# Performance work log

Measured on AMD Instinct MI355X. Metric: run time of the kernel, lower is better.

Reference implementation:

```python
import jax, jax.numpy as jnp
import numpy as np

DIM = 1024
INTER = 2048
N_EXPERTS = 8
TOP_K = 2
ROUTE_SCALE = 1.0


def setup_inputs() -> dict:
    key = jax.random.key(0)
    ks = jax.random.split(key, 4)
    x = jax.random.normal(ks[0], (4, 2048, DIM), dtype=jnp.float32)
    # Gate weight matches nn.Parameter(torch.randn(n_experts, dim))
    Wg = jax.random.normal(ks[1], (N_EXPERTS, DIM), dtype=jnp.float32)
    W1 = jax.random.normal(ks[2], (N_EXPERTS, DIM, INTER), dtype=jnp.float32) * (1.0 / np.sqrt(DIM))
    b1 = jnp.zeros((N_EXPERTS, INTER), dtype=jnp.float32)
    W2 = jax.random.normal(ks[3], (N_EXPERTS, INTER, DIM), dtype=jnp.float32) * (1.0 / np.sqrt(INTER))
    b2 = jnp.zeros((N_EXPERTS, DIM), dtype=jnp.float32)
    return {"x": x, "Wg": Wg, "W1": W1, "b1": b1, "W2": W2, "b2": b2}


def reference(x, Wg, W1, b1, W2, b2):
    # Flatten tokens: [T, D]
    xt = x.reshape(-1, DIM)
    T = xt.shape[0]

    # --- Gate: sigmoid scores, top-k, normalized weights ---
    scores = jax.nn.sigmoid(xt @ Wg.T)                       # [T, E]
    top_w, top_idx = jax.lax.top_k(scores, TOP_K)            # [T, K]
    top_w = top_w / jnp.sum(top_w, axis=-1, keepdims=True)
    top_w = top_w * ROUTE_SCALE

    # Sparse combine weights [T, E] (top_k indices are distinct per token)
    cw = jnp.zeros((T, N_EXPERTS), dtype=xt.dtype)
    cw = cw.at[jnp.arange(T)[:, None], top_idx].set(top_w)

    # --- Experts: dense per-expert MLP, weighted combine ---
    # (dropout is identity in eval mode)
    h = jax.nn.relu(jnp.einsum('td,edh->eth', xt, W1) + b1[:, None, :])   # [E, T, H]
    eo = jnp.einsum('eth,ehd->etd', h, W2) + b2[:, None, :]               # [E, T, D]
    y = jnp.einsum('etd,te->td', eo, cw)                                  # [T, D]
    return y
```

## Files before the change

### kernel.cpp

```cpp
#include <hip/hip_runtime.h>
#include <stdint.h>

#define DIM   1024
#define INTER 2048
#define NEXP  8
#define TIMAX 136

typedef _Float16 f16;
typedef __attribute__((ext_vector_type(2))) _Float16 f16x2;
typedef __attribute__((ext_vector_type(4))) _Float16 f16x4;
typedef __attribute__((ext_vector_type(8))) _Float16 f16x8;
typedef __attribute__((ext_vector_type(4))) float    f32x4;

static __device__ __forceinline__ void gload16(const void* gsrc, void* lds) {
    __builtin_amdgcn_global_load_lds(
        (const __attribute__((address_space(1))) uint32_t*)gsrc,
        (__attribute__((address_space(3))) uint32_t*)lds,
        16, 0, 0);
}

__device__ __forceinline__ void transpose_tile(const float* __restrict__ W, f16* __restrict__ Wt,
                                               int K, int N, int e, int kb, int nb, int t,
                                               f16 (*tile)[66]) {
    const float* We  = W  + (size_t)e * K * N;
    f16*         Wte = Wt + (size_t)e * K * N;
    const int kl = t >> 4;
    const int nq = t & 15;
    #pragma unroll
    for (int pass = 0; pass < 4; ++pass) {
        int k = pass * 16 + kl;
        float4 v = *(const float4*)&We[(size_t)(kb + k) * N + nb + nq * 4];
        f16x2 lo = { (f16)v.x, (f16)v.y };
        f16x2 hi = { (f16)v.z, (f16)v.w };
        *(f16x2*)&tile[k][nq * 4]     = lo;
        *(f16x2*)&tile[k][nq * 4 + 2] = hi;
    }
    __syncthreads();
    const int n  = t >> 2;
    const int kq = t & 3;
    f16x8 o0, o1;
    #pragma unroll
    for (int i = 0; i < 8; ++i) o0[i] = tile[kq * 16 + i][n];
    #pragma unroll
    for (int i = 0; i < 8; ++i) o1[i] = tile[kq * 16 + 8 + i][n];
    f16* dst = &Wte[(size_t)(nb + n) * K + kb + kq * 16];
    *(f16x8*)dst       = o0;
    *(f16x8*)(dst + 8) = o1;
}

__global__ void preprocess_kernel(const float* __restrict__ x, const float* __restrict__ Wg,
                                  const float* __restrict__ W1, const float* __restrict__ W2,
                                  f16* __restrict__ xh, f16* __restrict__ w1t, f16* __restrict__ w2t,
                                  float* __restrict__ gw, int* __restrict__ gidx, int T) {
    __shared__ f16 tile[64][66];
    const int bid     = blockIdx.x;
    const int NB_GATE = T / 4;
    const int NB_TR1  = (INTER / 64) * (DIM / 64) * NEXP;

    if (bid < NB_GATE) {
        const int tid  = threadIdx.x;
        const int tok  = bid * 4 + (tid >> 6);
        const int lane = tid & 63;
        const float4* xr  = (const float4*)(x + (size_t)tok * DIM);
        f16*          xhr = xh + (size_t)tok * DIM;
        float s[NEXP];
        #pragma unroll
        for (int e = 0; e < NEXP; ++e) s[e] = 0.f;
        #pragma unroll
        for (int it = 0; it < 4; ++it) {
            int i = it * 64 + lane;
            float4 xv = xr[i];
            f16x4 hv = { (f16)xv.x, (f16)xv.y, (f16)xv.z, (f16)xv.w };
            *(f16x4*)(xhr + i * 4) = hv;
            #pragma unroll
            for (int e = 0; e < NEXP; ++e) {
                float4 wv = ((const float4*)(Wg + e * DIM))[i];
                s[e] += xv.x * wv.x + xv.y * wv.y + xv.z * wv.z + xv.w * wv.w;
            }
        }
        #pragma unroll
        for (int e = 0; e < NEXP; ++e) {
            #pragma unroll
            for (int off = 32; off > 0; off >>= 1) s[e] += __shfl_xor(s[e], off);
        }
        if (lane == 0) {
            float sc[NEXP];
            #pragma unroll
            for (int e = 0; e < NEXP; ++e) sc[e] = 1.f / (1.f + expf(-s[e]));
            int i0 = 0;
            #pragma unroll
            for (int e = 1; e < NEXP; ++e) if (sc[e] > sc[i0]) i0 = e;
            int i1 = -1;
            #pragma unroll
            for (int e = 0; e < NEXP; ++e) if (e != i0 && (i1 < 0 || sc[e] > sc[i1])) i1 = e;
            float w0 = sc[i0], w1 = sc[i1];
            float inv = 1.f / (w0 + w1);
            gw[2 * tok + 0] = w0 * inv;
            gw[2 * tok + 1] = w1 * inv;
            gidx[2 * tok + 0] = i0;
            gidx[2 * tok + 1] = i1;
        }
    } else if (bid < NB_GATE + NB_TR1) {
        const int b  = bid - NB_GATE;
        const int nx = b % (INTER / 64);
        const int ky = (b / (INTER / 64)) % (DIM / 64);
        const int e  = b / ((INTER / 64) * (DIM / 64));
        transpose_tile(W1, w1t, DIM, INTER, e, ky * 64, nx * 64, threadIdx.x, tile);
    } else {
        const int b  = bid - NB_GATE - NB_TR1;
        const int nx = b % (DIM / 64);
        const int ky = (b / (DIM / 64)) % (INTER / 64);
        const int e  = b / ((DIM / 64) * (INTER / 64));
        transpose_tile(W2, w2t, INTER, DIM, e, ky * 64, nx * 64, threadIdx.x, tile);
    }
}

__global__ __launch_bounds__(1024)
void route_kernel(const int* __restrict__ gidx, const float* __restrict__ gw,
                  int* __restrict__ offsets, int* __restrict__ tor, float* __restrict__ gwp,
                  int* __restrict__ tileE, int* __restrict__ tileR0, int T) {
    const int tid  = threadIdx.x;
    const int lane = tid & 63;
    const int wv   = tid >> 6;
    const int NE   = 2 * T;
    __shared__ int wc[16][NEXP];
    __shared__ int rb[NEXP];

    int c[NEXP];
    #pragma unroll
    for (int e = 0; e < NEXP; ++e) c[e] = 0;
    for (int i = tid; i < NE; i += 1024) {
        int g = gidx[i];
        #pragma unroll
        for (int e = 0; e < NEXP; ++e) c[e] += (g == e) ? 1 : 0;
    }
    #pragma unroll
    for (int e = 0; e < NEXP; ++e) {
        #pragma unroll
        for (int off = 32; off > 0; off >>= 1) c[e] += __shfl_xor(c[e], off);
    }
    if (lane == 0) {
        #pragma unroll
        for (int e = 0; e < NEXP; ++e) wc[wv][e] = c[e];
    }
    __syncthreads();
    if (tid == 0) {
        int acc = 0;
        for (int e = 0; e < NEXP; ++e) {
            int t = 0;
            for (int w2 = 0; w2 < 16; ++w2) t += wc[w2][e];
            offsets[e] = acc;
            rb[e] = acc;
            acc += t;
        }
        offsets[NEXP] = acc;
        int nt = 0;
        for (int e = 0; e < NEXP; ++e)
            for (int r0 = offsets[e]; r0 < offsets[e + 1]; r0 += 128) {
                tileE[nt]  = e;
                tileR0[nt] = r0;
                ++nt;
            }
        for (; nt < TIMAX; ++nt) { tileE[nt] = -1; tileR0[nt] = 0; }
    }
    __syncthreads();

    for (int base = 0; base < NE; base += 1024) {
        int i = base + tid;
        int g = gidx[i];
        int myrank = 0;
        #pragma unroll
        for (int e = 0; e < NEXP; ++e) {
            unsigned long long m = __ballot(g == e);
            if (g == e) myrank = __popcll(m & ((1ull << lane) - 1ull));
            if (lane == 0) wc[wv][e] = __popcll(m);
        }
        __syncthreads();
        int pre = 0;
        for (int w2 = 0; w2 < wv; ++w2) pre += wc[w2][g];
        int pos = rb[g] + pre + myrank;
        tor[pos] = i >> 1;
        gwp[pos] = gw[i];
        __syncthreads();
        if (tid < NEXP) {
            int t = 0;
            for (int w2 = 0; w2 < 16; ++w2) t += wc[w2][tid];
            rb[tid] += t;
        }
        __syncthreads();
    }
}

template<int KD, int ND, bool RELU, bool GATHER, bool ATOMIC>
__global__ __launch_bounds__(256)
void moe_gemm_kernel(const f16* __restrict__ Abase, const f16* __restrict__ Bt,
                     const float* __restrict__ bias, const int* __restrict__ offsets,
                     const int* __restrict__ tok, const int* __restrict__ tileE,
                     const int* __restrict__ tileR0, const float* __restrict__ gwp,
                     float* __restrict__ yout, f16* __restrict__ Cout) {
    constexpr int NT  = ND / 128;
    constexpr int NT2 = NT / 2;
    const int bid = blockIdx.x;
    const int xcd = bid & 7;
    const int j   = bid >> 3;
    const int nt  = (j % NT2) * 2 + (xcd & 1);
    const int tih = j / NT2;
    const int ti  = tih * 4 + (xcd >> 1);

    const int e = tileE[ti];
    if (e < 0) return;
    const int row0   = tileR0[ti];
    const int rowEnd = offsets[e + 1];
    const int n0   = nt * 128;
    const int tid  = threadIdx.x;
    const int lane = tid & 63;
    const int wid  = tid >> 6;
    const int wr   = (wid >> 1) * 64;
    const int wc   = (wid & 1) * 64;

    __shared__ __align__(16) f16 As[128 * 64];
    __shared__ __align__(16) f16 Bs[128 * 64];

    const f16* Bte = Bt + (size_t)e * ND * KD;

    int aOff[4], bOff[4], ldsOff[4];
    #pragma unroll
    for (int i = 0; i < 4; ++i) {
        int c  = i * 256 + tid;
        int r  = c >> 3;
        int kc = (c & 7) ^ (r & 7);
        ldsOff[i] = c * 8;
        int gr = row0 + r;
        if (gr >= rowEnd) gr = rowEnd - 1;
        int ar = GATHER ? tok[gr] : gr;
        aOff[i] = ar * KD + kc * 8;
        bOff[i] = (n0 + r) * KD + kc * 8;
    }

    f32x4 acc[4][4] = {};

    const int rb    = lane & 15;
    const int jbase = lane >> 4;

    constexpr int nK = KD / 64;
    for (int kt = 0; kt < nK; ++kt) {
        const int k0 = kt * 64;
        #pragma unroll
        for (int i = 0; i < 4; ++i)
            gload16(Abase + (size_t)(aOff[i] + k0), &As[ldsOff[i]]);
        #pragma unroll
        for (int i = 0; i < 4; ++i)
            gload16(Bte + (size_t)(bOff[i] + k0), &Bs[ldsOff[i]]);
        __syncthreads();

        #pragma unroll
        for (int ks = 0; ks < 2; ++ks) {
            const int sl = (((ks * 4 + jbase) ^ (rb & 7))) * 8;
            f16x8 af[4], bfr[4];
            #pragma unroll
            for (int m = 0; m < 4; ++m)
                af[m] = *(const f16x8*)&As[(wr + m * 16 + rb) * 64 + sl];
            #pragma unroll
            for (int n = 0; n < 4; ++n)
                bfr[n] = *(const f16x8*)&Bs[(wc + n * 16 + rb) * 64 + sl];
            #pragma unroll
            for (int m = 0; m < 4; ++m)
                #pragma unroll
                for (int n = 0; n < 4; ++n)
                    acc[m][n] = __builtin_amdgcn_mfma_f32_16x16x32_f16(af[m], bfr[n], acc[m][n], 0, 0, 0);
        }

        __syncthreads();
    }

    const int rowsValid = rowEnd - row0;
    #pragma unroll
    for (int m = 0; m < 4; ++m) {
        #pragma unroll
        for (int n = 0; n < 4; ++n) {
            #pragma unroll
            for (int j2 = 0; j2 < 4; ++j2) {
                int rl  = wr + m * 16 + ((lane >> 4) << 2) + j2;
                int col = n0 + wc + n * 16 + (lane & 15);
                if (rl < rowsValid) {
                    int grow = row0 + rl;
                    float v = acc[m][n][j2] + bias[e * ND + col];
                    if (RELU) v = fmaxf(v, 0.f);
                    if (ATOMIC) {
                        atomicAdd(&yout[(size_t)tok[grow] * ND + col], v * gwp[grow]);
                    } else {
                        Cout[(size_t)grow * ND + col] = (f16)v;
                    }
                }
            }
        }
    }
}

extern "C" void kernel_launch(void* const* d_in, const int* in_sizes, int n_in,
                              void* d_out, int out_size, void* d_ws, size_t ws_size,
                              hipStream_t stream) {
    const float* x  = (const float*)d_in[0];
    const float* Wg = (const float*)d_in[1];
    const float* W1 = (const float*)d_in[2];
    const float* b1 = (const float*)d_in[3];
    const float* W2 = (const float*)d_in[4];
    const float* b2 = (const float*)d_in[5];
    float* y = (float*)d_out;
    const int T = in_sizes[0] / DIM;

    char* ws = (char*)d_ws;
    size_t off = 0;
    auto alloc = [&](size_t bytes) -> char* {
        char* p = ws + off;
        off += (bytes + 255) & ~(size_t)255;
        return p;
    };
    f16* xh   = (f16*)alloc((size_t)T * DIM * 2);
    f16* w1t  = (f16*)alloc((size_t)NEXP * DIM * INTER * 2);
    f16* w2t  = (f16*)alloc((size_t)NEXP * DIM * INTER * 2);
    f16* h    = (f16*)alloc((size_t)2 * T * INTER * 2);
    float* gw = (float*)alloc((size_t)T * 2 * 4);
    float* gwp= (float*)alloc((size_t)T * 2 * 4);
    int* gidx = (int*)alloc((size_t)T * 2 * 4);
    int* tor  = (int*)alloc((size_t)2 * T * 4);
    int* offsets = (int*)alloc(64 * 4);
    int* tileE   = (int*)alloc(TIMAX * 4);
    int* tileR0  = (int*)alloc(TIMAX * 4);

    hipMemsetAsync(y, 0, (size_t)T * DIM * 4, stream);

    const int NB_GATE = T / 4;
    const int NB_TR1  = (INTER / 64) * (DIM / 64) * NEXP;
    const int NB_TR2  = (DIM / 64) * (INTER / 64) * NEXP;
    preprocess_kernel<<<NB_GATE + NB_TR1 + NB_TR2, 256, 0, stream>>>(
        x, Wg, W1, W2, xh, w1t, w2t, gw, gidx, T);
    route_kernel<<<1, 1024, 0, stream>>>(gidx, gw, offsets, tor, gwp, tileE, tileR0, T);
    moe_gemm_kernel<DIM, INTER, true, true, false>
        <<<dim3((TIMAX / 4) * ((INTER / 128) / 2) * 8), 256, 0, stream>>>(
            xh, w1t, b1, offsets, tor, tileE, tileR0, nullptr, nullptr, h);
    moe_gemm_kernel<INTER, DIM, false, false, true>
        <<<dim3((TIMAX / 4) * ((DIM / 128) / 2) * 8), 256, 0, stream>>>(
            h, w2t, b2, offsets, tor, tileE, tileR0, gwp, y, nullptr);
}
```

Before: 375.4 us.

## Replace atomic scatter-add combine with f16 expert output and gather combine kernel

The second expert GEMM now writes per-row outputs as f16 to a buffer instead of doing float atomicAdds into y. A new combine kernel gathers each token's two expert rows using a reverse index from routing and writes y directly, so the memset is gone. This removes atomic contention and the memset, but adds an extra f16 intermediate buffer, another pass over it, and one more launch. Rounding the expert outputs to f16 before combining changes precision.

```diff
diff --git a/kernel.cpp b/kernel.cpp
--- a/kernel.cpp
+++ b/kernel.cpp
@@ -116,8 +116,8 @@
 }
 
 __global__ __launch_bounds__(1024)
-void route_kernel(const int* __restrict__ gidx, const float* __restrict__ gw,
-                  int* __restrict__ offsets, int* __restrict__ tor, float* __restrict__ gwp,
+void route_kernel(const int* __restrict__ gidx, int* __restrict__ offsets,
+                  int* __restrict__ tor, int* __restrict__ ros,
                   int* __restrict__ tileE, int* __restrict__ tileR0, int T) {
     const int tid  = threadIdx.x;
     const int lane = tid & 63;
@@ -180,7 +180,7 @@
         for (int w2 = 0; w2 < wv; ++w2) pre += wc[w2][g];
         int pos = rb[g] + pre + myrank;
         tor[pos] = i >> 1;
-        gwp[pos] = gw[i];
+        ros[i]   = pos;
         __syncthreads();
         if (tid < NEXP) {
             int t = 0;
@@ -191,13 +191,12 @@
     }
 }
 
-template<int KD, int ND, bool RELU, bool GATHER, bool ATOMIC>
+template<int KD, int ND, bool RELU, bool GATHER>
 __global__ __launch_bounds__(256)
 void moe_gemm_kernel(const f16* __restrict__ Abase, const f16* __restrict__ Bt,
                      const float* __restrict__ bias, const int* __restrict__ offsets,
                      const int* __restrict__ tok, const int* __restrict__ tileE,
-                     const int* __restrict__ tileR0, const float* __restrict__ gwp,
-                     float* __restrict__ yout, f16* __restrict__ Cout) {
+                     const int* __restrict__ tileR0, f16* __restrict__ Cout) {
     constexpr int NT  = ND / 128;
     constexpr int NT2 = NT / 2;
     const int bid = blockIdx.x;
@@ -283,18 +282,32 @@
                 int rl  = wr + m * 16 + ((lane >> 4) << 2) + j2;
                 int col = n0 + wc + n * 16 + (lane & 15);
                 if (rl < rowsValid) {
-                    int grow = row0 + rl;
                     float v = acc[m][n][j2] + bias[e * ND + col];
                     if (RELU) v = fmaxf(v, 0.f);
-                    if (ATOMIC) {
-                        atomicAdd(&yout[(size_t)tok[grow] * ND + col], v * gwp[grow]);
-                    } else {
-                        Cout[(size_t)grow * ND + col] = (f16)v;
-                    }
+                    Cout[(size_t)(row0 + rl) * ND + col] = (f16)v;
                 }
             }
         }
     }
+}
+
+__global__ void combine_kernel(const f16* __restrict__ eo, const int* __restrict__ ros,
+                               const float* __restrict__ gw, float* __restrict__ y, int T) {
+    int gid = blockIdx.x * 256 + threadIdx.x;
+    int t   = gid >> 7;
+    if (t >= T) return;
+    int c0 = (gid & 127) * 8;
+    int r0 = ros[2 * t], r1 = ros[2 * t + 1];
+    float w0 = gw[2 * t], w1 = gw[2 * t + 1];
+    f16x8 v0 = *(const f16x8*)(eo + (size_t)r0 * DIM + c0);
+    f16x8 v1 = *(const f16x8*)(eo + (size_t)r1 * DIM + c0);
+    f32x4 o0, o1;
+    #pragma unroll
+    for (int j = 0; j < 4; ++j) o0[j] = w0 * (float)v0[j] + w1 * (float)v1[j];
+    #pragma unroll
+    for (int j = 0; j < 4; ++j) o1[j] = w0 * (float)v0[4 + j] + w1 * (float)v1[4 + j];
+    *(f32x4*)(y + (size_t)t * DIM + c0)     = o0;
+    *(f32x4*)(y + (size_t)t * DIM + c0 + 4) = o1;
 }
 
 extern "C" void kernel_launch(void* const* d_in, const int* in_sizes, int n_in,
@@ -320,26 +333,26 @@
     f16* w1t  = (f16*)alloc((size_t)NEXP * DIM * INTER * 2);
     f16* w2t  = (f16*)alloc((size_t)NEXP * DIM * INTER * 2);
     f16* h    = (f16*)alloc((size_t)2 * T * INTER * 2);
+    f16* eo   = (f16*)alloc((size_t)2 * T * DIM * 2);
     float* gw = (float*)alloc((size_t)T * 2 * 4);
-    float* gwp= (float*)alloc((size_t)T * 2 * 4);
     int* gidx = (int*)alloc((size_t)T * 2 * 4);
+    int* ros  = (int*)alloc((size_t)T * 2 * 4);
     int* tor  = (int*)alloc((size_t)2 * T * 4);
     int* offsets = (int*)alloc(64 * 4);
     int* tileE   = (int*)alloc(TIMAX * 4);
     int* tileR0  = (int*)alloc(TIMAX * 4);
-
-    hipMemsetAsync(y, 0, (size_t)T * DIM * 4, stream);
 
     const int NB_GATE = T / 4;
     const int NB_TR1  = (INTER / 64) * (DIM / 64) * NEXP;
     const int NB_TR2  = (DIM / 64) * (INTER / 64) * NEXP;
     preprocess_kernel<<<NB_GATE + NB_TR1 + NB_TR2, 256, 0, stream>>>(
         x, Wg, W1, W2, xh, w1t, w2t, gw, gidx, T);
-    route_kernel<<<1, 1024, 0, stream>>>(gidx, gw, offsets, tor, gwp, tileE, tileR0, T);
-    moe_gemm_kernel<DIM, INTER, true, true, false>
+    route_kernel<<<1, 1024, 0, stream>>>(gidx, offsets, tor, ros, tileE, tileR0, T);
+    moe_gemm_kernel<DIM, INTER, true, true>
         <<<dim3((TIMAX / 4) * ((INTER / 128) / 2) * 8), 256, 0, stream>>>(
-            xh, w1t, b1, offsets, tor, tileE, tileR0, nullptr, nullptr, h);
-    moe_gemm_kernel<INTER, DIM, false, false, true>
+            xh, w1t, b1, offsets, tor, tileE, tileR0, h);
+    moe_gemm_kernel<INTER, DIM, false, false>
         <<<dim3((TIMAX / 4) * ((DIM / 128) / 2) * 8), 256, 0, stream>>>(
-            h, w2t, b2, offsets, tor, tileE, tileR0, gwp, y, nullptr);
-}
+            h, w2t, b2, offsets, tor, tileE, tileR0, eo);
+    combine_kernel<<<(T * DIM / 8 + 255) / 256, 256, 0, stream>>>(eo, ros, gw, y, T);
+}
```

Measured after the change: 319.5 us, median of 2. -14.9%, faster.
